# Kernel optimization log

Measured on AMD Instinct MI355X. Metric: run time of the kernel, lower is better.

Reference implementation:

```python
import jax, jax.numpy as jnp
import numpy as np

B, N, F_DIM, E, C = 8, 16384, 64, 262144, 10
BN_EPS = 1e-5


def setup_inputs() -> dict:
    key = jax.random.key(0)
    ks = jax.random.split(key, 10)
    s = 1.0 / np.sqrt(F_DIM)
    return {
        "x": jax.random.normal(ks[0], (B, N, F_DIM), jnp.float32),
        "edge_src": jax.random.randint(ks[1], (B, E), 0, N, jnp.int32),
        "edge_dst": jax.random.randint(ks[2], (B, E), 0, N, jnp.int32),
        "W1": jax.random.normal(ks[3], (F_DIM, F_DIM), jnp.float32) * s,
        "b1": jax.random.normal(ks[4], (F_DIM,), jnp.float32) * 0.01,
        "W2": jax.random.normal(ks[5], (F_DIM, F_DIM), jnp.float32) * s,
        "b2": jax.random.normal(ks[6], (F_DIM,), jnp.float32) * 0.01,
        "bn_gamma": jnp.ones((F_DIM,), jnp.float32),
        "bn_beta": jnp.zeros((F_DIM,), jnp.float32),
        "lin_W": jax.random.normal(ks[7], (C, N * F_DIM), jnp.float32) * (1.0 / np.sqrt(N * F_DIM)),
        "lin_b": jax.random.normal(ks[8], (C,), jnp.float32) * 0.01,
    }


def _graph_conv(x, src, dst, W, b):
    # DGL GraphConv, norm='both', in_feats == out_feats (aggregate-first path):
    # h = D_in^{-1/2} * A * (D_out^{-1/2} * x) @ W + b, degrees clamped to >= 1.
    ones = jnp.ones((src.shape[0],), x.dtype)
    deg_out = jnp.maximum(jax.ops.segment_sum(ones, src, num_segments=N), 1.0)
    deg_in = jnp.maximum(jax.ops.segment_sum(ones, dst, num_segments=N), 1.0)
    xs = x * jax.lax.rsqrt(deg_out)[:, None]          # [N, F]
    agg = jax.ops.segment_sum(xs[src], dst, num_segments=N)  # gather + scatter-add
    rst = agg * jax.lax.rsqrt(deg_in)[:, None]
    return rst @ W + b


def reference(x, edge_src, edge_dst, W1, b1, W2, b2, bn_gamma, bn_beta, lin_W, lin_b):
    conv = jax.vmap(_graph_conv, in_axes=(0, 0, 0, None, None))
    h = jax.nn.relu(conv(x, edge_src, edge_dst, W1, b1))  # conv1 + relu
    # dropout p=0.0 (eval): identity
    h = conv(h, edge_src, edge_dst, W2, b2)               # conv2 -> [B, N, F]
    # BatchNorm1d over channel F (torch normalizes over B and N in training mode)
    mean = jnp.mean(h, axis=(0, 1))
    var = jnp.var(h, axis=(0, 1))
    h = bn_gamma * (h - mean) * jax.lax.rsqrt(var + BN_EPS) + bn_beta
    flat = h.reshape(B, N * F_DIM)
    return flat @ lin_W.T + lin_b                         # [B, C]
```

## Files before the change

kernel.cpp:

```cpp
#include <hip/hip_runtime.h>

#define B_     8
#define N_     16384
#define F_     64
#define E_     262144
#define C_     10
#define NF_    (N_ * F_)
#define BN_    (B_ * N_)
#define BNF_   (B_ * N_ * F_)
#define BE_    (B_ * E_)
#define CAP_   48
#define CHUNK_ 8192
#define NCH_   (E_ / CHUNK_)
#define NW_    (N_ / 4)
#define NSB_   4096
#define NFB_   1024
#define EPS_   1e-5f

typedef _Float16 h8 __attribute__((ext_vector_type(8)));
typedef _Float16 h4 __attribute__((ext_vector_type(4)));
typedef float f32x4 __attribute__((ext_vector_type(4)));

#define SWZ(r, o) ((((r) * 64 + (o))) ^ (((r) & 7) << 3))

__global__ __launch_bounds__(256) void k_count(const int* __restrict__ src,
                                               const int* __restrict__ dst,
                                               unsigned int* __restrict__ partO,
                                               unsigned int* __restrict__ partI,
                                               const float* __restrict__ W1,
                                               const float* __restrict__ W2,
                                               _Float16* __restrict__ Wt1,
                                               _Float16* __restrict__ Wt2) {
    __shared__ unsigned int pO[NW_];
    __shared__ unsigned int pI[NW_];
    int t = threadIdx.x;
    if (blockIdx.x >= B_ * NCH_) {
        int g = blockIdx.x - B_ * NCH_;
        const float* Ws = (g & 8) ? W2 : W1;
        _Float16* Wd = (g & 8) ? Wt2 : Wt1;
        int c0 = (g & 7) * 512;
        for (int j = t; j < 512; j += 256) {
            int o = c0 + j;
            Wd[o] = (_Float16)Ws[(o & 63) * 64 + (o >> 6)];
        }
        return;
    }
    int b = blockIdx.x & 7, c = blockIdx.x >> 3;
    for (int i = t; i < NW_; i += 256) { pO[i] = 0; pI[i] = 0; }
    __syncthreads();
    const int4* sb = (const int4*)(src + (size_t)b * E_ + (size_t)c * CHUNK_);
    const int4* db = (const int4*)(dst + (size_t)b * E_ + (size_t)c * CHUNK_);
#pragma unroll
    for (int j = 0; j < CHUNK_ / 1024; ++j) {
        int4 s4 = sb[t + j * 256];
        int4 d4 = db[t + j * 256];
#pragma unroll
        for (int k = 0; k < 4; ++k) {
            int s = ((const int*)&s4)[k];
            int d = ((const int*)&d4)[k];
            atomicAdd(&pO[s >> 2], 1u << ((s & 3) * 8));
            atomicAdd(&pI[d >> 2], 1u << ((d & 3) * 8));
        }
    }
    __syncthreads();
    size_t base = (size_t)(b * NCH_ + c) * NW_;
    for (int i = t; i < NW_; i += 256) {
        partO[base + i] = pO[i];
        partI[base + i] = pI[i];
    }
}

__global__ __launch_bounds__(256) void k_offsets(const unsigned int* __restrict__ partO,
                                                 const unsigned int* __restrict__ partI,
                                                 unsigned int* __restrict__ baseArr,
                                                 float* __restrict__ degOr,
                                                 float* __restrict__ degIr,
                                                 int* __restrict__ cntI_g) {
    int gw = blockIdx.x * 256 + threadIdx.x;
    int b = gw >> 12;
    int rw = gw & 4095;
    unsigned int sumI = 0, sumO = 0;
    for (int c = 0; c < NCH_; ++c) {
        size_t idx = (size_t)(b * NCH_ + c) * NW_ + rw;
        unsigned int wI = partI[idx];
        baseArr[idx] = sumI;
        sumI += wI;
        sumO += partO[idx];
    }
    int row0 = gw * 4;
#pragma unroll
    for (int r = 0; r < 4; ++r) {
        unsigned int ci = (sumI >> (r * 8)) & 0xFFu;
        unsigned int co = (sumO >> (r * 8)) & 0xFFu;
        degIr[row0 + r] = rsqrtf(fmaxf((float)ci, 1.0f));
        degOr[row0 + r] = rsqrtf(fmaxf((float)co, 1.0f));
        cntI_g[row0 + r] = (int)ci;
    }
}

__global__ __launch_bounds__(256) void k_fill(const int* __restrict__ src,
                                              const int* __restrict__ dst,
                                              const unsigned int* __restrict__ baseArr,
                                              unsigned short* __restrict__ csr) {
    __shared__ unsigned int cur[NW_];
    __shared__ unsigned int bw[NW_];
    int t = threadIdx.x;
    int b = blockIdx.x & 7, c = blockIdx.x >> 3;
    size_t pbase = (size_t)(b * NCH_ + c) * NW_;
    for (int i = t; i < NW_; i += 256) { cur[i] = 0; bw[i] = baseArr[pbase + i]; }
    __syncthreads();
    const int4* sb = (const int4*)(src + (size_t)b * E_ + (size_t)c * CHUNK_);
    const int4* db = (const int4*)(dst + (size_t)b * E_ + (size_t)c * CHUNK_);
    unsigned short* cb = csr + (size_t)b * N_ * CAP_;
#pragma unroll
    for (int j = 0; j < CHUNK_ / 1024; ++j) {
        int4 s4 = sb[t + j * 256];
        int4 d4 = db[t + j * 256];
#pragma unroll
        for (int k = 0; k < 4; ++k) {
            int s = ((const int*)&s4)[k];
            int d = ((const int*)&d4)[k];
            unsigned int sh = (d & 3) * 8;
            unsigned int old = atomicAdd(&cur[d >> 2], 1u << sh);
            unsigned int pos = ((old >> sh) & 0xFFu) + ((bw[d >> 2] >> sh) & 0xFFu);
            if (pos < CAP_) cb[(size_t)d * CAP_ + pos] = (unsigned short)s;
        }
    }
}

template <bool IN16, bool SCALE>
__global__ __launch_bounds__(256) void k_mmf(const float* __restrict__ in32,
                                             const _Float16* __restrict__ in16,
                                             const _Float16* __restrict__ Wt,
                                             const float* __restrict__ rs,
                                             _Float16* __restrict__ out) {
    __shared__ _Float16 Al[4096];
    __shared__ _Float16 Bl[4096];
    int t = threadIdx.x;
    int bat = blockIdx.x & 7;
    int rowg = bat * N_ + (blockIdx.x >> 3) * 64;

#pragma unroll
    for (int j = 0; j < 2; ++j) {
        int c = t + j * 256;
        int r = c >> 3, o = (c & 7) * 8;
        *(h8*)&Al[SWZ(r, o)] = *(const h8*)(Wt + c * 8);
    }
#pragma unroll
    for (int j = 0; j < 2; ++j) {
        int c = t + j * 256;
        int r = c >> 3, o = (c & 7) * 8;
        h8 v;
        if constexpr (IN16) {
            v = *(const h8*)(in16 + (size_t)(rowg + r) * 64 + o);
        } else {
            const float4* p = (const float4*)(in32 + (size_t)(rowg + r) * 64 + o);
            float4 x0 = p[0], x1 = p[1];
            v[0] = (_Float16)x0.x; v[1] = (_Float16)x0.y;
            v[2] = (_Float16)x0.z; v[3] = (_Float16)x0.w;
            v[4] = (_Float16)x1.x; v[5] = (_Float16)x1.y;
            v[6] = (_Float16)x1.z; v[7] = (_Float16)x1.w;
        }
        *(h8*)&Bl[SWZ(r, o)] = v;
    }
    __syncthreads();

    int lane = t & 63;
    int w = t >> 6;
    int lm = lane & 15;
    int lk = (lane >> 4) * 8;
    f32x4 acc0 = {0.f, 0.f, 0.f, 0.f}, acc1 = {0.f, 0.f, 0.f, 0.f};
    f32x4 acc2 = {0.f, 0.f, 0.f, 0.f}, acc3 = {0.f, 0.f, 0.f, 0.f};
#pragma unroll
    for (int ks = 0; ks < 2; ++ks) {
        h8 a = *(const h8*)&Al[SWZ(w * 16 + lm, lk + ks * 32)];
        h8 vb0 = *(const h8*)&Bl[SWZ(0 + lm, lk + ks * 32)];
        h8 vb1 = *(const h8*)&Bl[SWZ(16 + lm, lk + ks * 32)];
        h8 vb2 = *(const h8*)&Bl[SWZ(32 + lm, lk + ks * 32)];
        h8 vb3 = *(const h8*)&Bl[SWZ(48 + lm, lk + ks * 32)];
        acc0 = __builtin_amdgcn_mfma_f32_16x16x32_f16(a, vb0, acc0, 0, 0, 0);
        acc1 = __builtin_amdgcn_mfma_f32_16x16x32_f16(a, vb1, acc1, 0, 0, 0);
        acc2 = __builtin_amdgcn_mfma_f32_16x16x32_f16(a, vb2, acc2, 0, 0, 0);
        acc3 = __builtin_amdgcn_mfma_f32_16x16x32_f16(a, vb3, acc3, 0, 0, 0);
    }
    int fo = w * 16 + (lane >> 4) * 4;
#define STORE_TILE(ACC, RT)                                                    \
    {                                                                          \
        int row = rowg + (RT) * 16 + lm;                                       \
        float scv = SCALE ? rs[row] : 1.0f;                                    \
        h4 ov;                                                                 \
        ov[0] = (_Float16)(ACC[0] * scv); ov[1] = (_Float16)(ACC[1] * scv);    \
        ov[2] = (_Float16)(ACC[2] * scv); ov[3] = (_Float16)(ACC[3] * scv);    \
        *(h4*)(out + (size_t)row * 64 + fo) = ov;                              \
    }
    STORE_TILE(acc0, 0)
    STORE_TILE(acc1, 1)
    STORE_TILE(acc2, 2)
    STORE_TILE(acc3, 3)
#undef STORE_TILE
}

template <bool CONV1>
__global__ __launch_bounds__(256, 6) void k_gat(
        const int* __restrict__ cnt, const unsigned short* __restrict__ csr,
        const _Float16* __restrict__ z, const float* __restrict__ degIr,
        const float* __restrict__ degOr, const float* __restrict__ bias,
        _Float16* __restrict__ out16, float* __restrict__ pstat) {
    __shared__ float sS[4][64];
    __shared__ float sQ[4][64];
    int t = threadIdx.x;
    int lane = t & 63;
    int wave = t >> 6;
    int c8 = lane & 7;
    int b = blockIdx.x & 7;
    int row = (blockIdx.x >> 3) * 32 + wave * 8 + (lane >> 3);
    int wid = b * N_ + row;
    const _Float16* zb = z + (size_t)b * NF_;
    int lb = lane & 56;
    int ho = c8 * 8;

    int n = cnt[wid];
    if (n > CAP_) n = CAP_;
    size_t cb = (size_t)wid * CAP_;
    uint4 ev = {0u, 0u, 0u, 0u};
    if (c8 < 6) ev = *(const uint4*)(csr + cb + c8 * 8);
    int m = n;
    m = max(m, __shfl_xor(m, 8));
    m = max(m, __shfl_xor(m, 16));
    m = max(m, __shfl_xor(m, 32));

    float af[8];
#pragma unroll
    for (int i = 0; i < 8; ++i) af[i] = 0.0f;

#define SEG(KOFF)                                                              \
    {                                                                          \
        int rem = n - (KOFF);                                                  \
        int srcl = lb + ((KOFF) >> 3);                                         \
        unsigned dd0 = __shfl(ev.x, srcl), dd1 = __shfl(ev.y, srcl);           \
        unsigned dd2 = __shfl(ev.z, srcl), dd3 = __shfl(ev.w, srcl);           \
        unsigned dd[4] = {dd0, dd1, dd2, dd3};                                 \
        h8 v[8];                                                               \
        _Pragma("unroll")                                                      \
        for (int jj = 0; jj < 8; ++jj) {                                       \
            int s = (int)((dd[jj >> 1] >> ((jj & 1) * 16)) & 0x3FFFu);         \
            h8 vv = {};                                                        \
            if (jj < rem) vv = *(const h8*)(zb + s * 64 + ho);                 \
            v[jj] = vv;                                                        \
        }                                                                      \
        h8 s0 = v[0] + v[1], s1 = v[2] + v[3];                                 \
        h8 s2 = v[4] + v[5], s3 = v[6] + v[7];                                 \
        h8 s4 = s0 + s1, s5 = s2 + s3;                                         \
        h8 s6 = s4 + s5;                                                       \
        _Pragma("unroll")                                                      \
        for (int i = 0; i < 8; ++i) af[i] += (float)s6[i];                     \
    }

    SEG(0)
    if (m > 8)  SEG(8)
    if (m > 16) SEG(16)
    if (m > 24) SEG(24)
    if (m > 32) SEG(32)
    if (m > 40) SEG(40)
#undef SEG

    float dIr = degIr[wid];
    float4 bv0 = *(const float4*)(bias + ho);
    float4 bv1 = *(const float4*)(bias + ho + 4);
    float bb[8] = {bv0.x, bv0.y, bv0.z, bv0.w, bv1.x, bv1.y, bv1.z, bv1.w};
    if constexpr (CONV1) {
        float po = degOr[wid];
        h8 ov;
#pragma unroll
        for (int i = 0; i < 8; ++i) {
            ov[i] = (_Float16)(fmaxf(fmaf(af[i], dIr, bb[i]), 0.0f) * po);
        }
        *(h8*)(out16 + (size_t)wid * 64 + ho) = ov;
    } else {
        float vv[8];
        h8 ov;
#pragma unroll
        for (int i = 0; i < 8; ++i) {
            vv[i] = fmaf(af[i], dIr, bb[i]);
            ov[i] = (_Float16)vv[i];
        }
        *(h8*)(out16 + (size_t)wid * 64 + ho) = ov;
        float ssv[8], qqv[8];
#pragma unroll
        for (int i = 0; i < 8; ++i) { ssv[i] = vv[i]; qqv[i] = vv[i] * vv[i]; }
#pragma unroll
        for (int i = 0; i < 8; ++i) {
            ssv[i] += __shfl_xor(ssv[i], 8);  qqv[i] += __shfl_xor(qqv[i], 8);
            ssv[i] += __shfl_xor(ssv[i], 16); qqv[i] += __shfl_xor(qqv[i], 16);
            ssv[i] += __shfl_xor(ssv[i], 32); qqv[i] += __shfl_xor(qqv[i], 32);
        }
        if (lane < 8) {
#pragma unroll
            for (int i = 0; i < 8; ++i) {
                sS[wave][lane * 8 + i] = ssv[i];
                sQ[wave][lane * 8 + i] = qqv[i];
            }
        }
        __syncthreads();
        if (t < 64) {
            float s_ = sS[0][t] + sS[1][t] + sS[2][t] + sS[3][t];
            float q_ = sQ[0][t] + sQ[1][t] + sQ[2][t] + sQ[3][t];
            pstat[(size_t)blockIdx.x * 128 + t] = s_;
            pstat[(size_t)blockIdx.x * 128 + 64 + t] = q_;
        }
    }
}

__global__ __launch_bounds__(256) void k_red(const float* __restrict__ part,
                                             float* __restrict__ stats2) {
    __shared__ float sred[256];
    int t = threadIdx.x;
    int half = t >> 7;
    int s = t & 127;
    int r0 = blockIdx.x * (NSB_ / 32);
    float acc = 0.0f;
    for (int k = 0; k < NSB_ / 32 / 2; ++k) {
        acc += part[(size_t)(r0 + k * 2 + half) * 128 + s];
    }
    sred[t] = acc;
    __syncthreads();
    if (t < 128) stats2[blockIdx.x * 128 + t] = sred[t] + sred[t + 128];
}

__global__ __launch_bounds__(256) void k_final(
        const _Float16* __restrict__ h, const float* __restrict__ linW,
        const float* __restrict__ stats2, const float* __restrict__ gamma,
        const float* __restrict__ beta, float* __restrict__ pf) {
    __shared__ float scs[64], shs[64];
    int t = threadIdx.x;
    if (t < 64) {
        float sum = 0.0f, sq = 0.0f;
#pragma unroll
        for (int j = 0; j < 32; ++j) {
            sum += stats2[j * 128 + t];
            sq  += stats2[j * 128 + 64 + t];
        }
        float inv = 1.0f / (float)BN_;
        float mean = sum * inv;
        float var  = sq * inv - mean * mean;
        float s = gamma[t] * rsqrtf(var + EPS_);
        scs[t] = s;
        shs[t] = beta[t] - mean * s;
    }
    __syncthreads();

    int lane = t & 63;
    int wv = t >> 6;
    int b0 = wv * 2, b1 = wv * 2 + 1;
    int base = blockIdx.x * (NF_ / NFB_);
    float4 s4  = *(const float4*)&scs[(lane & 15) * 4];
    float4 sh4 = *(const float4*)&shs[(lane & 15) * 4];
    float acc[C_][2];
#pragma unroll
    for (int c = 0; c < C_; ++c) { acc[c][0] = 0.0f; acc[c][1] = 0.0f; }

#pragma unroll
    for (int k = 0; k < 4; ++k) {
        int i = base + k * 256 + lane * 4;
        h4 ha = *(const h4*)(h + (size_t)b0 * NF_ + i);
        h4 hb = *(const h4*)(h + (size_t)b1 * NF_ + i);
        float h0[4], h1[4];
        h0[0] = fmaf((float)ha[0], s4.x, sh4.x);
        h0[1] = fmaf((float)ha[1], s4.y, sh4.y);
        h0[2] = fmaf((float)ha[2], s4.z, sh4.z);
        h0[3] = fmaf((float)ha[3], s4.w, sh4.w);
        h1[0] = fmaf((float)hb[0], s4.x, sh4.x);
        h1[1] = fmaf((float)hb[1], s4.y, sh4.y);
        h1[2] = fmaf((float)hb[2], s4.z, sh4.z);
        h1[3] = fmaf((float)hb[3], s4.w, sh4.w);
#pragma unroll
        for (int c = 0; c < C_; ++c) {
            float4 w4 = *(const float4*)(linW + (size_t)c * NF_ + i);
            float a0 = acc[c][0], a1 = acc[c][1];
            a0 = fmaf(h0[0], w4.x, a0); a0 = fmaf(h0[1], w4.y, a0);
            a0 = fmaf(h0[2], w4.z, a0); a0 = fmaf(h0[3], w4.w, a0);
            a1 = fmaf(h1[0], w4.x, a1); a1 = fmaf(h1[1], w4.y, a1);
            a1 = fmaf(h1[2], w4.z, a1); a1 = fmaf(h1[3], w4.w, a1);
            acc[c][0] = a0; acc[c][1] = a1;
        }
    }

#pragma unroll
    for (int c = 0; c < C_; ++c) {
#pragma unroll
        for (int j = 0; j < 2; ++j) {
            float v = acc[c][j];
            v += __shfl_down(v, 32);
            v += __shfl_down(v, 16);
            v += __shfl_down(v, 8);
            v += __shfl_down(v, 4);
            v += __shfl_down(v, 2);
            v += __shfl_down(v, 1);
            acc[c][j] = v;
        }
    }
    if (lane == 0) {
        float* p = pf + (size_t)blockIdx.x * 80;
#pragma unroll
        for (int c = 0; c < C_; ++c) {
            p[b0 * C_ + c] = acc[c][0];
            p[b1 * C_ + c] = acc[c][1];
        }
    }
}

__global__ __launch_bounds__(64) void k_fsum(const float* __restrict__ pf,
                                             const float* __restrict__ linb,
                                             float* __restrict__ out) {
    int o = blockIdx.x;
    int lane = threadIdx.x;
    float acc = 0.0f;
#pragma unroll
    for (int k = 0; k < 16; ++k) {
        acc += pf[(size_t)(k * 64 + lane) * 80 + o];
    }
    acc += __shfl_down(acc, 32);
    acc += __shfl_down(acc, 16);
    acc += __shfl_down(acc, 8);
    acc += __shfl_down(acc, 4);
    acc += __shfl_down(acc, 2);
    acc += __shfl_down(acc, 1);
    if (lane == 0) out[o] = acc + linb[o % C_];
}

extern "C" void kernel_launch(void* const* d_in, const int* in_sizes, int n_in,
                              void* d_out, int out_size, void* d_ws, size_t ws_size,
                              hipStream_t stream) {
    const float* x        = (const float*)d_in[0];
    const int*   edge_src = (const int*)d_in[1];
    const int*   edge_dst = (const int*)d_in[2];
    const float* W1       = (const float*)d_in[3];
    const float* b1       = (const float*)d_in[4];
    const float* W2       = (const float*)d_in[5];
    const float* b2       = (const float*)d_in[6];
    const float* gamma    = (const float*)d_in[7];
    const float* beta     = (const float*)d_in[8];
    const float* linW     = (const float*)d_in[9];
    const float* linb     = (const float*)d_in[10];
    float* out = (float*)d_out;

    char* w = (char*)d_ws;
    float* degOr = (float*)w;           w += BN_ * 4;
    float* degIr = (float*)w;           w += BN_ * 4;
    int*   cntI  = (int*)w;             w += BN_ * 4;
    unsigned short* csr = (unsigned short*)w; w += (size_t)BN_ * CAP_ * 2;
    _Float16* z    = (_Float16*)w;      w += (size_t)BNF_ * 2;
    _Float16* h1z  = (_Float16*)w;      w += (size_t)BNF_ * 2;
    _Float16* h2h  = (_Float16*)w;      w += (size_t)BNF_ * 2;
    unsigned int* partO   = (unsigned int*)w;  w += (size_t)B_ * NCH_ * NW_ * 4;
    unsigned int* partI   = (unsigned int*)w;  w += (size_t)B_ * NCH_ * NW_ * 4;
    unsigned int* baseArr = (unsigned int*)w;  w += (size_t)B_ * NCH_ * NW_ * 4;
    float* partStats = (float*)w;       w += (size_t)NSB_ * 128 * 4;
    float* stats2 = (float*)w;          w += 32 * 128 * 4;
    float* pf    = (float*)w;           w += (size_t)NFB_ * 80 * 4;
    _Float16* Wt1 = (_Float16*)w;       w += 4096 * 2;
    _Float16* Wt2 = (_Float16*)w;       w += 4096 * 2;

    k_count<<<B_ * NCH_ + 16, 256, 0, stream>>>(edge_src, edge_dst, partO, partI,
                                                W1, W2, Wt1, Wt2);
    k_offsets<<<BN_ / 4 / 256, 256, 0, stream>>>(partO, partI, baseArr, degOr, degIr, cntI);
    k_fill<<<B_ * NCH_, 256, 0, stream>>>(edge_src, edge_dst, baseArr, csr);

    k_mmf<false, true><<<BN_ / 64, 256, 0, stream>>>(x, nullptr, Wt1, degOr, z);
    k_gat<true><<<BN_ / 32, 256, 0, stream>>>(cntI, csr, z, degIr, degOr, b1, h1z, nullptr);

    k_mmf<true, false><<<BN_ / 64, 256, 0, stream>>>(nullptr, h1z, Wt2, nullptr, z);
    k_gat<false><<<BN_ / 32, 256, 0, stream>>>(cntI, csr, z, degIr, nullptr, b2, h2h, partStats);

    k_red<<<32, 256, 0, stream>>>(partStats, stats2);
    k_final<<<NFB_, 256, 0, stream>>>(h2h, linW, stats2, gamma, beta, pf);
    k_fsum<<<80, 64, 0, stream>>>(pf, linb, out);
}
```

Before: 227.6 us.

## Fuse conv1 aggregation with conv2 weight matmul into one kernel

The conv1 gather/aggregate kernel now multiplies its 32-row output tile by W2 with MFMA inside the same block, writing z2 directly. This removes the separate second k_mmf launch and the fp16 h1 round trip through global memory. The CSR edge load is also skipped for lanes beyond the node's edge count, and k_final splits the stats2 reduction across all threads instead of 64. The fused kernel adds LDS usage and a block barrier before the matmul, which may lower occupancy of the latency-bound gather phase.

```diff
diff --git a/kernel.cpp b/kernel.cpp
--- a/kernel.cpp
+++ b/kernel.cpp
@@ -200,40 +200,7 @@
 #undef STORE_TILE
 }
 
-template <bool CONV1>
-__global__ __launch_bounds__(256, 6) void k_gat(
-        const int* __restrict__ cnt, const unsigned short* __restrict__ csr,
-        const _Float16* __restrict__ z, const float* __restrict__ degIr,
-        const float* __restrict__ degOr, const float* __restrict__ bias,
-        _Float16* __restrict__ out16, float* __restrict__ pstat) {
-    __shared__ float sS[4][64];
-    __shared__ float sQ[4][64];
-    int t = threadIdx.x;
-    int lane = t & 63;
-    int wave = t >> 6;
-    int c8 = lane & 7;
-    int b = blockIdx.x & 7;
-    int row = (blockIdx.x >> 3) * 32 + wave * 8 + (lane >> 3);
-    int wid = b * N_ + row;
-    const _Float16* zb = z + (size_t)b * NF_;
-    int lb = lane & 56;
-    int ho = c8 * 8;
-
-    int n = cnt[wid];
-    if (n > CAP_) n = CAP_;
-    size_t cb = (size_t)wid * CAP_;
-    uint4 ev = {0u, 0u, 0u, 0u};
-    if (c8 < 6) ev = *(const uint4*)(csr + cb + c8 * 8);
-    int m = n;
-    m = max(m, __shfl_xor(m, 8));
-    m = max(m, __shfl_xor(m, 16));
-    m = max(m, __shfl_xor(m, 32));
-
-    float af[8];
-#pragma unroll
-    for (int i = 0; i < 8; ++i) af[i] = 0.0f;
-
-#define SEG(KOFF)                                                              \
+#define GAT_SEG(KOFF)                                                          \
     {                                                                          \
         int rem = n - (KOFF);                                                  \
         int srcl = lb + ((KOFF) >> 3);                                         \
@@ -256,58 +223,159 @@
         for (int i = 0; i < 8; ++i) af[i] += (float)s6[i];                     \
     }
 
-    SEG(0)
-    if (m > 8)  SEG(8)
-    if (m > 16) SEG(16)
-    if (m > 24) SEG(24)
-    if (m > 32) SEG(32)
-    if (m > 40) SEG(40)
-#undef SEG
+__global__ __launch_bounds__(256, 6) void k_gmm(
+        const int* __restrict__ cnt, const unsigned short* __restrict__ csr,
+        const _Float16* __restrict__ z, const float* __restrict__ degIr,
+        const float* __restrict__ degOr, const float* __restrict__ bias,
+        const _Float16* __restrict__ Wt2, _Float16* __restrict__ out) {
+    __shared__ _Float16 Al[4096];
+    __shared__ _Float16 Bl[2048];
+    int t = threadIdx.x;
+    int lane = t & 63;
+    int wave = t >> 6;
+    int c8 = lane & 7;
+    int b = blockIdx.x & 7;
+    int rl = wave * 8 + (lane >> 3);
+    int row0 = (blockIdx.x >> 3) * 32;
+    int wid = b * N_ + row0 + rl;
+    const _Float16* zb = z + (size_t)b * NF_;
+    int lb = lane & 56;
+    int ho = c8 * 8;
+
+#pragma unroll
+    for (int j = 0; j < 2; ++j) {
+        int c = t + j * 256;
+        int r = c >> 3, o = (c & 7) * 8;
+        *(h8*)&Al[SWZ(r, o)] = *(const h8*)(Wt2 + c * 8);
+    }
+
+    int n = cnt[wid];
+    if (n > CAP_) n = CAP_;
+    size_t cb = (size_t)wid * CAP_;
+    uint4 ev = {0u, 0u, 0u, 0u};
+    if (c8 * 8 < n) ev = *(const uint4*)(csr + cb + c8 * 8);
+    int m = n;
+    m = max(m, __shfl_xor(m, 8));
+    m = max(m, __shfl_xor(m, 16));
+    m = max(m, __shfl_xor(m, 32));
+
+    float af[8];
+#pragma unroll
+    for (int i = 0; i < 8; ++i) af[i] = 0.0f;
+    GAT_SEG(0)
+    if (m > 8)  GAT_SEG(8)
+    if (m > 16) GAT_SEG(16)
+    if (m > 24) GAT_SEG(24)
+    if (m > 32) GAT_SEG(32)
+    if (m > 40) GAT_SEG(40)
+
+    float dIr = degIr[wid];
+    float po = degOr[wid];
+    float4 bv0 = *(const float4*)(bias + ho);
+    float4 bv1 = *(const float4*)(bias + ho + 4);
+    float bb[8] = {bv0.x, bv0.y, bv0.z, bv0.w, bv1.x, bv1.y, bv1.z, bv1.w};
+    h8 ov;
+#pragma unroll
+    for (int i = 0; i < 8; ++i) {
+        ov[i] = (_Float16)(fmaxf(fmaf(af[i], dIr, bb[i]), 0.0f) * po);
+    }
+    *(h8*)&Bl[SWZ(rl, ho)] = ov;
+    __syncthreads();
+
+    int lm = lane & 15;
+    int lk = (lane >> 4) * 8;
+    f32x4 acc0 = {0.f, 0.f, 0.f, 0.f}, acc1 = {0.f, 0.f, 0.f, 0.f};
+#pragma unroll
+    for (int ks = 0; ks < 2; ++ks) {
+        h8 a  = *(const h8*)&Al[SWZ(wave * 16 + lm, lk + ks * 32)];
+        h8 v0 = *(const h8*)&Bl[SWZ(lm, lk + ks * 32)];
+        h8 v1 = *(const h8*)&Bl[SWZ(16 + lm, lk + ks * 32)];
+        acc0 = __builtin_amdgcn_mfma_f32_16x16x32_f16(a, v0, acc0, 0, 0, 0);
+        acc1 = __builtin_amdgcn_mfma_f32_16x16x32_f16(a, v1, acc1, 0, 0, 0);
+    }
+    int fo = wave * 16 + (lane >> 4) * 4;
+    int rowg = b * N_ + row0;
+    h4 o0, o1;
+    o0[0] = (_Float16)acc0[0]; o0[1] = (_Float16)acc0[1];
+    o0[2] = (_Float16)acc0[2]; o0[3] = (_Float16)acc0[3];
+    o1[0] = (_Float16)acc1[0]; o1[1] = (_Float16)acc1[1];
+    o1[2] = (_Float16)acc1[2]; o1[3] = (_Float16)acc1[3];
+    *(h4*)(out + (size_t)(rowg + lm) * 64 + fo) = o0;
+    *(h4*)(out + (size_t)(rowg + 16 + lm) * 64 + fo) = o1;
+}
+
+__global__ __launch_bounds__(256, 6) void k_gat(
+        const int* __restrict__ cnt, const unsigned short* __restrict__ csr,
+        const _Float16* __restrict__ z, const float* __restrict__ degIr,
+        const float* __restrict__ bias, _Float16* __restrict__ out16,
+        float* __restrict__ pstat) {
+    __shared__ float sS[4][64];
+    __shared__ float sQ[4][64];
+    int t = threadIdx.x;
+    int lane = t & 63;
+    int wave = t >> 6;
+    int c8 = lane & 7;
+    int b = blockIdx.x & 7;
+    int row = (blockIdx.x >> 3) * 32 + wave * 8 + (lane >> 3);
+    int wid = b * N_ + row;
+    const _Float16* zb = z + (size_t)b * NF_;
+    int lb = lane & 56;
+    int ho = c8 * 8;
+
+    int n = cnt[wid];
+    if (n > CAP_) n = CAP_;
+    size_t cb = (size_t)wid * CAP_;
+    uint4 ev = {0u, 0u, 0u, 0u};
+    if (c8 * 8 < n) ev = *(const uint4*)(csr + cb + c8 * 8);
+    int m = n;
+    m = max(m, __shfl_xor(m, 8));
+    m = max(m, __shfl_xor(m, 16));
+    m = max(m, __shfl_xor(m, 32));
+
+    float af[8];
+#pragma unroll
+    for (int i = 0; i < 8; ++i) af[i] = 0.0f;
+    GAT_SEG(0)
+    if (m > 8)  GAT_SEG(8)
+    if (m > 16) GAT_SEG(16)
+    if (m > 24) GAT_SEG(24)
+    if (m > 32) GAT_SEG(32)
+    if (m > 40) GAT_SEG(40)
 
     float dIr = degIr[wid];
     float4 bv0 = *(const float4*)(bias + ho);
     float4 bv1 = *(const float4*)(bias + ho + 4);
     float bb[8] = {bv0.x, bv0.y, bv0.z, bv0.w, bv1.x, bv1.y, bv1.z, bv1.w};
-    if constexpr (CONV1) {
-        float po = degOr[wid];
-        h8 ov;
+    float vv[8];
+    h8 ov;
+#pragma unroll
+    for (int i = 0; i < 8; ++i) {
+        vv[i] = fmaf(af[i], dIr, bb[i]);
+        ov[i] = (_Float16)vv[i];
+    }
+    *(h8*)(out16 + (size_t)wid * 64 + ho) = ov;
+    float ssv[8], qqv[8];
+#pragma unroll
+    for (int i = 0; i < 8; ++i) { ssv[i] = vv[i]; qqv[i] = vv[i] * vv[i]; }
+#pragma unroll
+    for (int i = 0; i < 8; ++i) {
+        ssv[i] += __shfl_xor(ssv[i], 8);  qqv[i] += __shfl_xor(qqv[i], 8);
+        ssv[i] += __shfl_xor(ssv[i], 16); qqv[i] += __shfl_xor(qqv[i], 16);
+        ssv[i] += __shfl_xor(ssv[i], 32); qqv[i] += __shfl_xor(qqv[i], 32);
+    }
+    if (lane < 8) {
 #pragma unroll
         for (int i = 0; i < 8; ++i) {
-            ov[i] = (_Float16)(fmaxf(fmaf(af[i], dIr, bb[i]), 0.0f) * po);
-        }
-        *(h8*)(out16 + (size_t)wid * 64 + ho) = ov;
-    } else {
-        float vv[8];
-        h8 ov;
-#pragma unroll
-        for (int i = 0; i < 8; ++i) {
-            vv[i] = fmaf(af[i], dIr, bb[i]);
-            ov[i] = (_Float16)vv[i];
-        }
-        *(h8*)(out16 + (size_t)wid * 64 + ho) = ov;
-        float ssv[8], qqv[8];
-#pragma unroll
-        for (int i = 0; i < 8; ++i) { ssv[i] = vv[i]; qqv[i] = vv[i] * vv[i]; }
-#pragma unroll
-        for (int i = 0; i < 8; ++i) {
-            ssv[i] += __shfl_xor(ssv[i], 8);  qqv[i] += __shfl_xor(qqv[i], 8);
-            ssv[i] += __shfl_xor(ssv[i], 16); qqv[i] += __shfl_xor(qqv[i], 16);
-            ssv[i] += __shfl_xor(ssv[i], 32); qqv[i] += __shfl_xor(qqv[i], 32);
-        }
-        if (lane < 8) {
-#pragma unroll
-            for (int i = 0; i < 8; ++i) {
-                sS[wave][lane * 8 + i] = ssv[i];
-                sQ[wave][lane * 8 + i] = qqv[i];
-            }
-        }
-        __syncthreads();
-        if (t < 64) {
-            float s_ = sS[0][t] + sS[1][t] + sS[2][t] + sS[3][t];
-            float q_ = sQ[0][t] + sQ[1][t] + sQ[2][t] + sQ[3][t];
-            pstat[(size_t)blockIdx.x * 128 + t] = s_;
-            pstat[(size_t)blockIdx.x * 128 + 64 + t] = q_;
-        }
+            sS[wave][lane * 8 + i] = ssv[i];
+            sQ[wave][lane * 8 + i] = qqv[i];
+        }
+    }
+    __syncthreads();
+    if (t < 64) {
+        float s_ = sS[0][t] + sS[1][t] + sS[2][t] + sS[3][t];
+        float q_ = sQ[0][t] + sQ[1][t] + sQ[2][t] + sQ[3][t];
+        pstat[(size_t)blockIdx.x * 128 + t] = s_;
+        pstat[(size_t)blockIdx.x * 128 + 64 + t] = q_;
     }
 }
 
@@ -331,15 +399,20 @@
         const _Float16* __restrict__ h, const float* __restrict__ linW,
         const float* __restrict__ stats2, const float* __restrict__ gamma,
         const float* __restrict__ beta, float* __restrict__ pf) {
+    __shared__ float pre[256];
     __shared__ float scs[64], shs[64];
     int t = threadIdx.x;
+    {
+        int u = t & 127, jh = t >> 7;
+        float a = 0.0f;
+#pragma unroll
+        for (int j = 0; j < 16; ++j) a += stats2[(jh * 16 + j) * 128 + u];
+        pre[t] = a;
+    }
+    __syncthreads();
     if (t < 64) {
-        float sum = 0.0f, sq = 0.0f;
-#pragma unroll
-        for (int j = 0; j < 32; ++j) {
-            sum += stats2[j * 128 + t];
-            sq  += stats2[j * 128 + 64 + t];
-        }
+        float sum = pre[t] + pre[t + 128];
+        float sq  = pre[t + 64] + pre[t + 192];
         float inv = 1.0f / (float)BN_;
         float mean = sum * inv;
         float var  = sq * inv - mean * mean;
@@ -449,8 +522,8 @@
     float* degIr = (float*)w;           w += BN_ * 4;
     int*   cntI  = (int*)w;             w += BN_ * 4;
     unsigned short* csr = (unsigned short*)w; w += (size_t)BN_ * CAP_ * 2;
-    _Float16* z    = (_Float16*)w;      w += (size_t)BNF_ * 2;
-    _Float16* h1z  = (_Float16*)w;      w += (size_t)BNF_ * 2;
+    _Float16* z1   = (_Float16*)w;      w += (size_t)BNF_ * 2;
+    _Float16* z2   = (_Float16*)w;      w += (size_t)BNF_ * 2;
     _Float16* h2h  = (_Float16*)w;      w += (size_t)BNF_ * 2;
     unsigned int* partO   = (unsigned int*)w;  w += (size_t)B_ * NCH_ * NW_ * 4;
     unsigned int* partI   = (unsigned int*)w;  w += (size_t)B_ * NCH_ * NW_ * 4;
@@ -466,11 +539,9 @@
     k_offsets<<<BN_ / 4 / 256, 256, 0, stream>>>(partO, partI, baseArr, degOr, degIr, cntI);
     k_fill<<<B_ * NCH_, 256, 0, stream>>>(edge_src, edge_dst, baseArr, csr);
 
-    k_mmf<false, true><<<BN_ / 64, 256, 0, stream>>>(x, nullptr, Wt1, degOr, z);
-    k_gat<true><<<BN_ / 32, 256, 0, stream>>>(cntI, csr, z, degIr, degOr, b1, h1z, nullptr);
-
-    k_mmf<true, false><<<BN_ / 64, 256, 0, stream>>>(nullptr, h1z, Wt2, nullptr, z);
-    k_gat<false><<<BN_ / 32, 256, 0, stream>>>(cntI, csr, z, degIr, nullptr, b2, h2h, partStats);
+    k_mmf<false, true><<<BN_ / 64, 256, 0, stream>>>(x, nullptr, Wt1, degOr, z1);
+    k_gmm<<<BN_ / 32, 256, 0, stream>>>(cntI, csr, z1, degIr, degOr, b1, Wt2, z2);
+    k_gat<<<BN_ / 32, 256, 0, stream>>>(cntI, csr, z2, degIr, b2, h2h, partStats);
 
     k_red<<<32, 256, 0, stream>>>(partStats, stats2);
     k_final<<<NFB_, 256, 0, stream>>>(h2h, linW, stats2, gamma, beta, pf);
```

New measurement: 228.3 us. About the same (+0.3%).
